# Performance work log

Hardware: AMD Instinct MI355X
Metric: run time of the kernel (lower is better)

Reference implementation:

```python
import jax, jax.numpy as jnp
import numpy as np

B, S, D, H = 2, 4096, 512, 8
DK = D // H  # 64


def setup_inputs() -> dict:
    key = jax.random.key(0)
    ks = jax.random.split(key, 7)
    scale = 1.0 / np.sqrt(D)
    return {
        "query": jax.random.normal(ks[0], (B, S, D), dtype=jnp.float32),
        "key": jax.random.normal(ks[1], (B, S, D), dtype=jnp.float32),
        "value": jax.random.normal(ks[2], (B, S, D), dtype=jnp.float32),
        # nn.Linear weights, stored [out, in] as in torch; y = x @ W.T
        "Wq": jax.random.normal(ks[3], (D, D), dtype=jnp.float32) * scale,
        "Wk": jax.random.normal(ks[4], (D, D), dtype=jnp.float32) * scale,
        "Wv": jax.random.normal(ks[5], (D, D), dtype=jnp.float32) * scale,
        "Wo": jax.random.normal(ks[6], (D, D), dtype=jnp.float32) * scale,
    }


def reference(query, key, value, Wq, Wk, Wv, Wo):
    # projections (torch Linear: x @ W.T)
    q = query @ Wq.T  # [B,S,D]
    k = key @ Wk.T
    v = value @ Wv.T
    # split heads -> [B,H,S,DK]
    q = q.reshape(B, S, H, DK).transpose(0, 2, 1, 3)
    k = k.reshape(B, S, H, DK).transpose(0, 2, 1, 3)
    v = v.reshape(B, S, H, DK).transpose(0, 2, 1, 3)
    # scores [B,H,S,S], softmax, weighted sum (dropout=0 / eval)
    scores = jnp.einsum("bhqd,bhkd->bhqk", q, k) / np.sqrt(DK).astype(np.float32)
    weights = jax.nn.softmax(scores, axis=-1)
    attn = jnp.einsum("bhqk,bhkd->bhqd", weights, v)  # [B,H,S,DK]
    # merge heads -> [B,S,D], output projection
    out = attn.transpose(0, 2, 1, 3).reshape(B, S, D)
    return out @ Wo.T
```

## Files before the change

kernel.cpp:

```cpp
#include <hip/hip_runtime.h>
#include <hip/hip_bf16.h>

typedef short short8 __attribute__((ext_vector_type(8)));
typedef short short4v __attribute__((ext_vector_type(4)));
typedef float floatx4 __attribute__((ext_vector_type(4)));
typedef unsigned int uint4v __attribute__((ext_vector_type(4)));

constexpr int Bc = 2, Sc = 4096, Dc = 512, Hc = 8, DKc = 64;
constexpr int Mc = Bc * Sc;

static __device__ __forceinline__ unsigned short f2bf(float f) {
  unsigned int u = __builtin_bit_cast(unsigned int, f);
  unsigned int rb = ((u >> 16) & 1u) + 0x7fffu;
  return (unsigned short)((u + rb) >> 16);
}
static __device__ __forceinline__ unsigned int cvt_pk_bf16(float lo, float hi) {
  unsigned int r;
  asm("v_cvt_pk_bf16_f32 %0, %1, %2" : "=v"(r) : "v"(lo), "v"(hi));
  return r;
}
static __device__ __forceinline__ float exp2_fast(float x) {
  float r;
  asm("v_exp_f32 %0, %1" : "=v"(r) : "v"(x));
  return r;
}

template <int IN_F32, int OUT_F32, int W_F32, int VT_OUT>
static __device__ __forceinline__ void gemm_body(
    const void* __restrict__ Xv, const void* __restrict__ Wp,
    void* __restrict__ Yv, const int N, const int K) {
  constexpr int BM = 128, BN = 64, BK = 32, LDP = 40;
  __shared__ unsigned short As[2][BM * LDP];
  __shared__ unsigned short Bs[2][BN * LDP];
  const int tid = threadIdx.x;
  const int lane = tid & 63, wid = tid >> 6;
  const int wm = wid >> 1, wn = wid & 1;
  const int bm = blockIdx.y * BM, bn = blockIdx.x * BN;
  const int rq = lane & 15, lg = lane >> 4, kk8 = lg * 8;
  const int sr = tid >> 1, sc = (tid & 1) * 16;
  const int brow = tid >> 2, bc8 = (tid & 3) * 8;

  floatx4 acc[4][2] = {};

  float a32[16];
  short8 a16[2];
  float b32[8];
  short8 b16;

  auto load_tile = [&](int k0) {
    if (IN_F32) {
      const float* src = (const float*)Xv + (size_t)(bm + sr) * K + k0 + sc;
#pragma unroll
      for (int i = 0; i < 4; ++i) {
        float4 v = *(const float4*)(src + i * 4);
        a32[4 * i + 0] = v.x; a32[4 * i + 1] = v.y;
        a32[4 * i + 2] = v.z; a32[4 * i + 3] = v.w;
      }
    } else {
      const unsigned short* src =
          (const unsigned short*)Xv + (size_t)(bm + sr) * K + k0 + sc;
      a16[0] = *(const short8*)src;
      a16[1] = *(const short8*)(src + 8);
    }
    if (W_F32) {
      const float* wsrc = (const float*)Wp + (size_t)(bn + brow) * K + k0 + bc8;
#pragma unroll
      for (int i = 0; i < 2; ++i) {
        float4 v = *(const float4*)(wsrc + i * 4);
        b32[4 * i + 0] = v.x; b32[4 * i + 1] = v.y;
        b32[4 * i + 2] = v.z; b32[4 * i + 3] = v.w;
      }
    } else {
      b16 = *(const short8*)((const unsigned short*)Wp +
                             (size_t)(bn + brow) * K + k0 + bc8);
    }
  };
  auto store_tile = [&](int bf) {
    if (IN_F32) {
      unsigned int t2[8];
#pragma unroll
      for (int i = 0; i < 8; ++i) t2[i] = cvt_pk_bf16(a32[2 * i], a32[2 * i + 1]);
      uint4v u0 = {t2[0], t2[1], t2[2], t2[3]};
      uint4v u1 = {t2[4], t2[5], t2[6], t2[7]};
      *(uint4v*)&As[bf][sr * LDP + sc] = u0;
      *(uint4v*)&As[bf][sr * LDP + sc + 8] = u1;
    } else {
      *(short8*)&As[bf][sr * LDP + sc] = a16[0];
      *(short8*)&As[bf][sr * LDP + sc + 8] = a16[1];
    }
    if (W_F32) {
      unsigned int t2[4];
#pragma unroll
      for (int i = 0; i < 4; ++i) t2[i] = cvt_pk_bf16(b32[2 * i], b32[2 * i + 1]);
      uint4v u = {t2[0], t2[1], t2[2], t2[3]};
      *(uint4v*)&Bs[bf][brow * LDP + bc8] = u;
    } else {
      *(short8*)&Bs[bf][brow * LDP + bc8] = b16;
    }
  };

  load_tile(0);
  store_tile(0);

  const int NK = K / BK;
  for (int it = 0; it < NK; ++it) {
    const int cur = it & 1;
    __syncthreads();

    if (it < NK - 1) load_tile((it + 1) * BK);

    short8 af[4], bfr[2];
#pragma unroll
    for (int mi = 0; mi < 4; ++mi)
      af[mi] = *(const short8*)&As[cur][(wm * 64 + mi * 16 + rq) * LDP + kk8];
#pragma unroll
    for (int ni = 0; ni < 2; ++ni)
      bfr[ni] = *(const short8*)&Bs[cur][(wn * 32 + ni * 16 + rq) * LDP + kk8];
#pragma unroll
    for (int mi = 0; mi < 4; ++mi)
#pragma unroll
      for (int ni = 0; ni < 2; ++ni)
        acc[mi][ni] = __builtin_amdgcn_mfma_f32_16x16x32_bf16(
            af[mi], bfr[ni], acc[mi][ni], 0, 0, 0);

    if (it < NK - 1) store_tile(cur ^ 1);
  }

  if (VT_OUT) {
    __syncthreads();
    unsigned short* T = (unsigned short*)As;
    const int bb = bm >> 12;
    const int sl0 = bm & 4095;
#pragma unroll
    for (int mi = 0; mi < 4; ++mi) {
      const int spb = wm * 64 + (mi >> 1) * 32 + lg * 8 + (mi & 1) * 4;
#pragma unroll
      for (int ni = 0; ni < 2; ++ni) {
        const int c = wn * 32 + ni * 16 + rq;
#pragma unroll
        for (int j = 0; j < 4; ++j)
          T[c * 136 + spb + j] = f2bf(acc[mi][ni][j]);
      }
    }
    __syncthreads();
    const int c = tid >> 2, seg = (tid & 3) * 32;
    unsigned short* dst = (unsigned short*)Yv +
        ((size_t)bb * Dc + bn + c) * Sc + sl0 + seg;
#pragma unroll
    for (int u = 0; u < 4; ++u)
      *(short8*)(dst + u * 8) = *(const short8*)&T[c * 136 + seg + u * 8];
  } else {
#pragma unroll
    for (int mi = 0; mi < 4; ++mi)
#pragma unroll
      for (int ni = 0; ni < 2; ++ni)
#pragma unroll
        for (int j = 0; j < 4; ++j) {
          int r = bm + wm * 64 + mi * 16 + lg * 4 + j;
          int c = bn + wn * 32 + ni * 16 + rq;
          float v = acc[mi][ni][j];
          if (OUT_F32)
            ((float*)Yv)[(size_t)r * N + c] = v;
          else
            ((unsigned short*)Yv)[(size_t)r * N + c] = f2bf(v);
        }
  }
}

__global__ __launch_bounds__(256) void gemm_qkv(
    const float* __restrict__ xq, const float* __restrict__ xk,
    const float* __restrict__ xv, const float* __restrict__ wq,
    const float* __restrict__ wk, const float* __restrict__ wv,
    unsigned short* __restrict__ yq, unsigned short* __restrict__ yk,
    unsigned short* __restrict__ vt) {
  const int z = blockIdx.z;
  if (z == 2) {
    gemm_body<1, 0, 1, 1>(xv, wv, vt, Dc, Dc);
  } else {
    const float* X = (z == 0) ? xq : xk;
    const float* W = (z == 0) ? wq : wk;
    unsigned short* Y = (z == 0) ? yq : yk;
    gemm_body<1, 0, 1, 0>(X, W, Y, Dc, Dc);
  }
}

__global__ __launch_bounds__(256) void gemm_out(
    const unsigned short* __restrict__ x, const float* __restrict__ w,
    float* __restrict__ y) {
  gemm_body<0, 1, 1, 0>(x, w, y, Dc, Dc);
}

__global__ __launch_bounds__(512, 4) void attn_fwd(
    const unsigned short* __restrict__ Qp, const unsigned short* __restrict__ Kp,
    const unsigned short* __restrict__ Vtp, unsigned short* __restrict__ Op) {
  __shared__ unsigned char smem[33792];
  unsigned short* KsB = (unsigned short*)smem;
  unsigned short* VsB = (unsigned short*)(smem + 16384);

  const int tid = threadIdx.x, lane = tid & 63, wid = tid >> 6;
  const int qc = wid >> 1, kh = wid & 1;
  const int F = blockIdx.y * 32 + blockIdx.x;
  const int L = (F & 7) * 64 + (F >> 3);
  const int bh = L >> 5, qt = L & 31;
  const int b = bh >> 3, h = bh & 7;
  const int q0 = qt * 128 + qc * 32;
  const int rq = lane & 15, lg = lane >> 4, kk8 = lg * 8;

  const unsigned short* Qb = Qp + ((size_t)b * Sc) * Dc + h * DKc;
  const unsigned short* Kb = Kp + ((size_t)b * Sc) * Dc + h * DKc;
  const unsigned short* Vh = Vtp + ((size_t)b * Dc + h * DKc) * Sc;

  short8 qa[2][2];
#pragma unroll
  for (int qi = 0; qi < 2; ++qi)
#pragma unroll
    for (int c = 0; c < 2; ++c)
      qa[qi][c] = *(const short8*)(Qb + (size_t)(q0 + qi * 16 + rq) * Dc + c * 32 + kk8);

  floatx4 o_acc[2][4] = {};
  floatx4 acc_l[2] = {};
  float m_run[2] = {-1e30f, -1e30f};

  short8 ones;
#pragma unroll
  for (int j = 0; j < 8; ++j) ones[j] = (short)0x3F80;

  const float C2 = 0.18033688f;
  const float THR = 8.0f;

  const int sr = tid >> 3, sc8 = (tid & 7) * 8;
  const int st = (sr * 64 + sc8) ^ ((sr & 7) << 3);
  const int sx = (rq & 7) << 3;

  short8 kr = *(const short8*)(Kb + (size_t)sr * Dc + sc8);
  short8 vr = *(const short8*)(Vh + (size_t)sr * Sc + sc8);
  *(short8*)&KsB[st] = kr;
  *(short8*)&VsB[st] = vr;

  for (int it = 0; it < 64; ++it) {
    const int cur = it & 1;
    __syncthreads();

    if (it < 63) {
      const int kn = (it + 1) * 64;
      kr = *(const short8*)(Kb + (size_t)(kn + sr) * Dc + sc8);
      vr = *(const short8*)(Vh + (size_t)sr * Sc + kn + sc8);
    }

    const unsigned short* Ks = KsB + cur * 4096;
    const unsigned short* Vs = VsB + cur * 4096;

    short8 ka[2][2];
#pragma unroll
    for (int ks = 0; ks < 2; ++ks)
#pragma unroll
      for (int c = 0; c < 2; ++c) {
        const int row = kh * 32 + ks * 16 + rq;
        ka[ks][c] = *(const short8*)&Ks[(row * 64 + c * 32 + kk8) ^ sx];
      }

    short8 pb_[2];
#pragma unroll
    for (int qi = 0; qi < 2; ++qi) {
      floatx4 s[2] = {};
#pragma unroll
      for (int ks = 0; ks < 2; ++ks) {
        s[ks] = __builtin_amdgcn_mfma_f32_16x16x32_bf16(ka[ks][0], qa[qi][0], s[ks], 0, 0, 0);
        s[ks] = __builtin_amdgcn_mfma_f32_16x16x32_bf16(ka[ks][1], qa[qi][1], s[ks], 0, 0, 0);
      }
      float t1 = fmaxf(fmaxf(s[0][0], s[0][1]), s[0][2]);
      float t2 = fmaxf(fmaxf(s[0][3], s[1][0]), s[1][1]);
      float t3 = fmaxf(fmaxf(s[1][2], s[1][3]), t1);
      float tp = fmaxf(t3, t2) * C2;

      if (__any(tp > m_run[qi] + THR)) {
        float tm = tp;
        tm = fmaxf(tm, __shfl_xor(tm, 16, 64));
        tm = fmaxf(tm, __shfl_xor(tm, 32, 64));
        if (__any(tm > m_run[qi])) {
          float mn = fmaxf(m_run[qi], tm);
          float scf = exp2_fast(m_run[qi] - mn);
          m_run[qi] = mn;
          float sc_c[4];
#pragma unroll
          for (int j = 0; j < 4; ++j) sc_c[j] = __shfl(scf, lg * 4 + j, 64);
#pragma unroll
          for (int j = 0; j < 4; ++j) {
            acc_l[qi][j] *= sc_c[j];
#pragma unroll
            for (int dt = 0; dt < 4; ++dt) o_acc[qi][dt][j] *= sc_c[j];
          }
        }
      }

      const float lm = m_run[qi];
      unsigned int pw0, pw1, pw2, pw3;
      {
        float p0 = exp2_fast(fmaf(s[0][0], C2, -lm));
        float p1 = exp2_fast(fmaf(s[0][1], C2, -lm));
        float p2 = exp2_fast(fmaf(s[0][2], C2, -lm));
        float p3 = exp2_fast(fmaf(s[0][3], C2, -lm));
        pw0 = cvt_pk_bf16(p0, p1);
        pw1 = cvt_pk_bf16(p2, p3);
      }
      {
        float p0 = exp2_fast(fmaf(s[1][0], C2, -lm));
        float p1 = exp2_fast(fmaf(s[1][1], C2, -lm));
        float p2 = exp2_fast(fmaf(s[1][2], C2, -lm));
        float p3 = exp2_fast(fmaf(s[1][3], C2, -lm));
        pw2 = cvt_pk_bf16(p0, p1);
        pw3 = cvt_pk_bf16(p2, p3);
      }
      uint4v pw = {pw0, pw1, pw2, pw3};
      pb_[qi] = __builtin_bit_cast(short8, pw);
    }

#pragma unroll
    for (int dt = 0; dt < 4; ++dt) {
      const int vrow = dt * 16 + rq;
      short8 v = *(const short8*)&Vs[(vrow * 64 + kh * 32 + kk8) ^ sx];
      o_acc[0][dt] = __builtin_amdgcn_mfma_f32_16x16x32_bf16(pb_[0], v, o_acc[0][dt], 0, 0, 0);
      o_acc[1][dt] = __builtin_amdgcn_mfma_f32_16x16x32_bf16(pb_[1], v, o_acc[1][dt], 0, 0, 0);
    }
    acc_l[0] = __builtin_amdgcn_mfma_f32_16x16x32_bf16(pb_[0], ones, acc_l[0], 0, 0, 0);
    acc_l[1] = __builtin_amdgcn_mfma_f32_16x16x32_bf16(pb_[1], ones, acc_l[1], 0, 0, 0);

    if (it < 63) {
      *(short8*)&KsB[(cur ^ 1) * 4096 + st] = kr;
      *(short8*)&VsB[(cur ^ 1) * 4096 + st] = vr;
    }
  }

  __syncthreads();
  float* MO = (float*)smem;
  float* ML = (float*)(smem + 32768);
  if (kh == 1) {
#pragma unroll
    for (int qi = 0; qi < 2; ++qi) {
#pragma unroll
      for (int j = 0; j < 4; ++j) {
        int row = qc * 32 + qi * 16 + lg * 4 + j;
        if (rq == 0) ML[row * 2 + 1] = acc_l[qi][j];
#pragma unroll
        for (int dt = 0; dt < 4; ++dt)
          MO[(size_t)row * 64 + dt * 16 + rq] = o_acc[qi][dt][j];
      }
      if (lg == 0) ML[(qc * 32 + qi * 16 + rq) * 2] = m_run[qi];
    }
  }
  __syncthreads();
  if (kh == 0) {
#pragma unroll
    for (int qi = 0; qi < 2; ++qi) {
      float m0c[4];
#pragma unroll
      for (int j = 0; j < 4; ++j) m0c[j] = __shfl(m_run[qi], lg * 4 + j, 64);
#pragma unroll
      for (int j = 0; j < 4; ++j) {
        int row = qc * 32 + qi * 16 + lg * 4 + j;
        int r = q0 + qi * 16 + lg * 4 + j;
        float m1 = ML[row * 2 + 0], l1 = ML[row * 2 + 1];
        float mx = fmaxf(m0c[j], m1);
        float a0 = exp2_fast(m0c[j] - mx), a1 = exp2_fast(m1 - mx);
        float inv = 1.0f / (acc_l[qi][j] * a0 + l1 * a1);
#pragma unroll
        for (int dt = 0; dt < 4; ++dt) {
          float o = (o_acc[qi][dt][j] * a0 + MO[(size_t)row * 64 + dt * 16 + rq] * a1) * inv;
          Op[((size_t)b * Sc + r) * Dc + h * DKc + dt * 16 + rq] = f2bf(o);
        }
      }
    }
  }
}

extern "C" void kernel_launch(void* const* d_in, const int* in_sizes, int n_in,
                              void* d_out, int out_size, void* d_ws, size_t ws_size,
                              hipStream_t stream) {
  const float* q_in = (const float*)d_in[0];
  const float* k_in = (const float*)d_in[1];
  const float* v_in = (const float*)d_in[2];
  const float* Wq = (const float*)d_in[3];
  const float* Wk = (const float*)d_in[4];
  const float* Wv = (const float*)d_in[5];
  const float* Wo = (const float*)d_in[6];

  unsigned short* qb = (unsigned short*)d_ws;
  unsigned short* kb = qb + (size_t)Mc * Dc;
  unsigned short* ab = kb + (size_t)Mc * Dc;
  unsigned short* vt = ab + (size_t)Mc * Dc;

  dim3 gq(Dc / 64, Mc / 128, 3);
  gemm_qkv<<<gq, 256, 0, stream>>>(q_in, k_in, v_in, Wq, Wk, Wv, qb, kb, vt);

  dim3 ga(Sc / 128, Bc * Hc);
  attn_fwd<<<ga, 512, 0, stream>>>(qb, kb, vt, ab);

  dim3 gg(Dc / 64, Mc / 128);
  gemm_out<<<gg, 256, 0, stream>>>(ab, Wo, (float*)d_out);
}
```

Measured before the change: 162.9 us.

## Load K and V tiles directly from global into registers, drop LDS staging

The attention loop no longer stages K and V tiles through double-buffered shared memory with per-iteration barriers. Each wave now loads its own K fragments straight from global memory into registers, ping-ponged across two register sets, and loads V fragments directly before the PV MFMAs. This removes the __syncthreads, LDS writes and reads, but the two query-chunk waves sharing a key half now fetch the same K/V data redundantly from global/L2. It also issues uncoalesced strided 16-byte loads and uses more registers.

```diff
diff --git a/kernel.cpp b/kernel.cpp
--- a/kernel.cpp
+++ b/kernel.cpp
@@ -194,8 +194,6 @@
     const unsigned short* __restrict__ Qp, const unsigned short* __restrict__ Kp,
     const unsigned short* __restrict__ Vtp, unsigned short* __restrict__ Op) {
   __shared__ unsigned char smem[33792];
-  unsigned short* KsB = (unsigned short*)smem;
-  unsigned short* VsB = (unsigned short*)(smem + 16384);
 
   const int tid = threadIdx.x, lane = tid & 63, wid = tid >> 6;
   const int qc = wid >> 1, kh = wid & 1;
@@ -210,6 +208,9 @@
   const unsigned short* Kb = Kp + ((size_t)b * Sc) * Dc + h * DKc;
   const unsigned short* Vh = Vtp + ((size_t)b * Dc + h * DKc) * Sc;
 
+  const unsigned short* Kw = Kb + (size_t)(kh * 32 + rq) * Dc + kk8;
+  const unsigned short* Vw = Vh + (size_t)rq * Sc + kh * 32 + kk8;
+
   short8 qa[2][2];
 #pragma unroll
   for (int qi = 0; qi < 2; ++qi)
@@ -228,36 +229,19 @@
   const float C2 = 0.18033688f;
   const float THR = 8.0f;
 
-  const int sr = tid >> 3, sc8 = (tid & 7) * 8;
-  const int st = (sr * 64 + sc8) ^ ((sr & 7) << 3);
-  const int sx = (rq & 7) << 3;
-
-  short8 kr = *(const short8*)(Kb + (size_t)sr * Dc + sc8);
-  short8 vr = *(const short8*)(Vh + (size_t)sr * Sc + sc8);
-  *(short8*)&KsB[st] = kr;
-  *(short8*)&VsB[st] = vr;
-
-  for (int it = 0; it < 64; ++it) {
-    const int cur = it & 1;
-    __syncthreads();
-
-    if (it < 63) {
-      const int kn = (it + 1) * 64;
-      kr = *(const short8*)(Kb + (size_t)(kn + sr) * Dc + sc8);
-      vr = *(const short8*)(Vh + (size_t)sr * Sc + kn + sc8);
-    }
-
-    const unsigned short* Ks = KsB + cur * 4096;
-    const unsigned short* Vs = VsB + cur * 4096;
-
-    short8 ka[2][2];
+  auto load_k = [&](short8 (&ka)[2][2], int k0) {
 #pragma unroll
     for (int ks = 0; ks < 2; ++ks)
 #pragma unroll
-      for (int c = 0; c < 2; ++c) {
-        const int row = kh * 32 + ks * 16 + rq;
-        ka[ks][c] = *(const short8*)&Ks[(row * 64 + c * 32 + kk8) ^ sx];
-      }
+      for (int c = 0; c < 2; ++c)
+        ka[ks][c] = *(const short8*)(Kw + (size_t)(k0 + ks * 16) * Dc + c * 32);
+  };
+
+  auto compute = [&](short8 (&ka)[2][2], int k0) {
+    short8 vv[4];
+#pragma unroll
+    for (int dt = 0; dt < 4; ++dt)
+      vv[dt] = *(const short8*)(Vw + (size_t)(dt * 16) * Sc + k0);
 
     short8 pb_[2];
 #pragma unroll
@@ -317,18 +301,20 @@
 
 #pragma unroll
     for (int dt = 0; dt < 4; ++dt) {
-      const int vrow = dt * 16 + rq;
-      short8 v = *(const short8*)&Vs[(vrow * 64 + kh * 32 + kk8) ^ sx];
-      o_acc[0][dt] = __builtin_amdgcn_mfma_f32_16x16x32_bf16(pb_[0], v, o_acc[0][dt], 0, 0, 0);
-      o_acc[1][dt] = __builtin_amdgcn_mfma_f32_16x16x32_bf16(pb_[1], v, o_acc[1][dt], 0, 0, 0);
+      o_acc[0][dt] = __builtin_amdgcn_mfma_f32_16x16x32_bf16(pb_[0], vv[dt], o_acc[0][dt], 0, 0, 0);
+      o_acc[1][dt] = __builtin_amdgcn_mfma_f32_16x16x32_bf16(pb_[1], vv[dt], o_acc[1][dt], 0, 0, 0);
     }
     acc_l[0] = __builtin_amdgcn_mfma_f32_16x16x32_bf16(pb_[0], ones, acc_l[0], 0, 0, 0);
     acc_l[1] = __builtin_amdgcn_mfma_f32_16x16x32_bf16(pb_[1], ones, acc_l[1], 0, 0, 0);
-
-    if (it < 63) {
-      *(short8*)&KsB[(cur ^ 1) * 4096 + st] = kr;
-      *(short8*)&VsB[(cur ^ 1) * 4096 + st] = vr;
-    }
+  };
+
+  short8 kaA[2][2], kaB[2][2];
+  load_k(kaA, 0);
+  for (int it = 0; it < 64; it += 2) {
+    load_k(kaB, (it + 1) * 64);
+    compute(kaA, it * 64);
+    if (it + 2 < 64) load_k(kaA, (it + 2) * 64);
+    compute(kaB, (it + 1) * 64);
   }
 
   __syncthreads();
```

Measured after the change: 418.6 us. 157% more time.
